# Optimization experiments

Measured on AMD Instinct MI355X. Metric: run time of the kernel, lower is better.

## Reference

```python
import jax, jax.numpy as jnp
import numpy as np

EMBED_DIM = 512
KDIM = 64
VDIM = 64


def setup_inputs() -> dict:
    key = jax.random.key(0)
    kx, kq, kk, kv = jax.random.split(key, 4)
    B, S = 4, 4096
    x = jax.random.normal(kx, (B, S, EMBED_DIM), dtype=jnp.float32)
    # nn.Linear(embed_dim, out) weight has shape [out, embed_dim]
    WQ = jax.random.normal(kq, (KDIM, EMBED_DIM), dtype=jnp.float32) * (EMBED_DIM ** -0.5)
    WK = jax.random.normal(kk, (KDIM, EMBED_DIM), dtype=jnp.float32) * (EMBED_DIM ** -0.5)
    WV = jax.random.normal(kv, (VDIM, EMBED_DIM), dtype=jnp.float32) * (EMBED_DIM ** -0.5)
    return {"x": x, "WQ": WQ, "WK": WK, "WV": WV}


def reference(x, WQ, WK, WV):
    # q,k: [B,S,kdim]; v: [B,S,vdim] (self-attention: x[0] is x[-1])
    q = jnp.einsum('bse,ke->bsk', x, WQ)
    k = jnp.einsum('bse,ke->bsk', x, WK)
    v = jnp.einsum('bse,ve->bsv', x, WV)
    scale = k.shape[-1] ** -0.5
    scores = jnp.einsum('bqk,bsk->bqs', q, k) * scale  # [B,S,S]
    # dropout p=0.0 -> identity; masked branch in source is a no-op (non-in-place masked_fill discarded)
    attn = jax.nn.softmax(scores, axis=-1)
    out = jnp.einsum('bqs,bsv->bqv', attn, v)  # [B,S,vdim]
    return out
```

## Files before the change

kernel.cpp:

```cpp
#include <hip/hip_runtime.h>

#define BATCH 4
#define SEQ   4096
#define EMB   512
#define HD    64

typedef __attribute__((ext_vector_type(8))) short short8;
typedef __attribute__((ext_vector_type(4))) float floatx4;

static __device__ __forceinline__ unsigned short f2bf(float f) {
  unsigned u = __builtin_bit_cast(unsigned, f);
  u += 0x7fffu + ((u >> 16) & 1u);
  return (unsigned short)(u >> 16);
}
static __device__ __forceinline__ float bf2f(unsigned short h) {
  unsigned u = ((unsigned)h) << 16;
  return __builtin_bit_cast(float, u);
}
static __device__ __forceinline__ unsigned pack_hi16(float lo, float hi) {
#if __has_builtin(__builtin_amdgcn_perm)
  return __builtin_amdgcn_perm(__builtin_bit_cast(unsigned, hi),
                               __builtin_bit_cast(unsigned, lo), 0x07060302u);
#else
  return (__builtin_bit_cast(unsigned, lo) >> 16) |
         (__builtin_bit_cast(unsigned, hi) & 0xffff0000u);
#endif
}
static __device__ __forceinline__ unsigned pack_f16(float a, float b) {
#if __has_builtin(__builtin_amdgcn_cvt_pkrtz)
  typedef __fp16 fp16v2 __attribute__((ext_vector_type(2)));
  fp16v2 h = __builtin_amdgcn_cvt_pkrtz(a, b);
  return __builtin_bit_cast(unsigned, h);
#else
  _Float16 ha = (_Float16)a, hb = (_Float16)b;
  return (unsigned)__builtin_bit_cast(unsigned short, ha) |
         ((unsigned)__builtin_bit_cast(unsigned short, hb) << 16);
#endif
}
static __device__ __forceinline__ float f16_to_f32(unsigned short bits) {
  _Float16 h = __builtin_bit_cast(_Float16, bits);
  return (float)h;
}

__global__ __launch_bounds__(256) void convw_kernel(
    const float* __restrict__ WQ, const float* __restrict__ WK,
    const float* __restrict__ WV, unsigned short* __restrict__ Wpk)
{
  int t = blockIdx.x * 256 + threadIdx.x;
  int p    = t >> 12;
  int w    = (t >> 10) & 3;
  int kc   = (t >> 6) & 15;
  int lane = t & 63;
  int lr = lane & 15, g = lane >> 4;
  const float* src = (p == 0) ? WQ : ((p == 1) ? WK : WV);
  const float4* s4 = (const float4*)(src + (16 * w + lr) * EMB + kc * 32 + 8 * g);
  float4 a = s4[0], b = s4[1];
  float vv[8] = {a.x, a.y, a.z, a.w, b.x, b.y, b.z, b.w};
  short8 o;
#pragma unroll
  for (int j = 0; j < 8; ++j) {
    unsigned short h = f2bf(vv[j]);
    o[j] = (p == 3) ? (short)f2bf(vv[j] - bf2f(h)) : (short)h;
  }
  *(short8*)(Wpk + (size_t)t * 8) = o;
}

__global__ __launch_bounds__(256) void proj_kernel(
    const float* __restrict__ x,
    const unsigned short* __restrict__ Wpk,
    unsigned short* __restrict__ Qb,
    unsigned short* __restrict__ Kb,
    unsigned short* __restrict__ VTb)
{
  const int tid  = threadIdx.x;
  const int lane = tid & 63;
  const int w    = tid >> 6;
  const int lr   = lane & 15, g = lane >> 4;
  const long rowBase = (long)blockIdx.x * 32;

  const float* xp[2];
  xp[0] = x + (rowBase + lr) * EMB + 8 * g;
  xp[1] = x + (rowBase + 16 + lr) * EMB + 8 * g;
  const unsigned short* const wb0 = Wpk + (size_t)(w * 16) * 512 + lane * 8;

  floatx4 accQ[2], accK[2], accV[2];
#pragma unroll
  for (int rt = 0; rt < 2; ++rt) {
    floatx4 z = {0.f, 0.f, 0.f, 0.f};
    accQ[rt] = z; accK[rt] = z; accV[rt] = z;
  }

#pragma unroll 4
  for (int kc = 0; kc < 16; ++kc) {
    const unsigned short* wb = wb0 + kc * 512;
    short8 wq  = *(const short8*)(wb);
    short8 wk  = *(const short8*)(wb + 32768);
    short8 wvh = *(const short8*)(wb + 2 * 32768);
    short8 wvl = *(const short8*)(wb + 3 * 32768);
#pragma unroll
    for (int rt = 0; rt < 2; ++rt) {
      const float4* p = (const float4*)(xp[rt] + kc * 32);
      float4 a = p[0], b = p[1];
      float vv[8] = {a.x, a.y, a.z, a.w, b.x, b.y, b.z, b.w};
      short8 xh, xl;
#pragma unroll
      for (int i = 0; i < 8; ++i) {
        unsigned short h = f2bf(vv[i]);
        xh[i] = (short)h;
        xl[i] = (short)f2bf(vv[i] - bf2f(h));
      }
      accQ[rt] = __builtin_amdgcn_mfma_f32_16x16x32_bf16(wq, xh, accQ[rt], 0, 0, 0);
      accK[rt] = __builtin_amdgcn_mfma_f32_16x16x32_bf16(wk, xh, accK[rt], 0, 0, 0);
      accV[rt] = __builtin_amdgcn_mfma_f32_16x16x32_bf16(xh, wvh, accV[rt], 0, 0, 0);
      accV[rt] = __builtin_amdgcn_mfma_f32_16x16x32_bf16(xl, wvh, accV[rt], 0, 0, 0);
      accV[rt] = __builtin_amdgcn_mfma_f32_16x16x32_bf16(xh, wvl, accV[rt], 0, 0, 0);
    }
  }

  const int bb  = (int)(rowBase >> 12);
  const int sIn = (int)(rowBase & 4095);
#pragma unroll
  for (int rt = 0; rt < 2; ++rt) {
    {
      long row = rowBase + 16 * rt + lr;
      int  col = 16 * w + 4 * g;
      ushort4 u; u.x = f2bf(accQ[rt][0]); u.y = f2bf(accQ[rt][1]);
      u.z = f2bf(accQ[rt][2]); u.w = f2bf(accQ[rt][3]);
      *(ushort4*)(Qb + row * HD + col) = u;
      ushort4 v; v.x = f2bf(accK[rt][0]); v.y = f2bf(accK[rt][1]);
      v.z = f2bf(accK[rt][2]); v.w = f2bf(accK[rt][3]);
      *(ushort4*)(Kb + row * HD + col) = v;
    }
    {
      long addr = ((long)(bb * 64 + 16 * w + lr)) * SEQ + sIn + 16 * rt + 4 * g;
      ushort4 u; u.x = f2bf(accV[rt][0]); u.y = f2bf(accV[rt][1]);
      u.z = f2bf(accV[rt][2]); u.w = f2bf(accV[rt][3]);
      *(ushort4*)(VTb + addr) = u;
    }
  }
}

#define PST 72

__global__ __launch_bounds__(256, 2) void flash_kernel(
    const unsigned short* __restrict__ Qb,
    const unsigned short* __restrict__ Kb,
    const unsigned short* __restrict__ VTb,
    unsigned short* __restrict__ Opart,
    float* __restrict__ Lpart)
{
  __shared__ __align__(16) unsigned short K0lds[64 * 64];
  __shared__ __align__(16) unsigned short V0lds[64 * 64];
  __shared__ __align__(16) unsigned short K1lds[64 * 64];
  __shared__ __align__(16) unsigned short V1lds[64 * 64];
  __shared__ __align__(16) unsigned short Plds[4][64 * PST];

  const int tid  = threadIdx.x;
  const int lane = tid & 63;
  const int w    = tid >> 6;
  const int lr   = lane & 15, g = lane >> 4;
  const int qb   = blockIdx.x >> 3;
  const int ks   = blockIdx.x & 7;
  const int bb   = qb >> 4;
  const long qrow0 = (long)qb * 256 + 64 * w;
  const int  kbase = ks * 512;

  const int koff0 = lr * 64 + 8 * ((    g) ^ (lr & 7));
  const int koff1 = lr * 64 + 8 * ((4 + g) ^ (lr & 7));
  const int voff0 = koff0, voff1 = koff1;
  const int pwoff = lr * PST + 4 * g;
  const int proff = lr * PST + 8 * g;
  unsigned short* const pw = &Plds[w][0];

  const int ci0  = tid;
  const int row0 = ci0 >> 3,        cc0 = (ci0 & 7) ^ (row0 & 7);
  const int ci1  = 256 + tid;
  const int row1 = ci1 >> 3,        cc1 = (ci1 & 7) ^ (row1 & 7);
  const unsigned short* const gK0 = Kb  + ((long)bb * SEQ + kbase + row0) * HD + cc0 * 8;
  const unsigned short* const gK1 = Kb  + ((long)bb * SEQ + kbase + row1) * HD + cc1 * 8;
  const unsigned short* const gV0 = VTb + ((long)bb * HD + row0) * SEQ + kbase + cc0 * 8;
  const unsigned short* const gV1 = VTb + ((long)bb * HD + row1) * SEQ + kbase + cc1 * 8;

  short8 qf[4][2];
#pragma unroll
  for (int qh = 0; qh < 4; ++qh)
#pragma unroll
    for (int ec = 0; ec < 2; ++ec)
      qf[qh][ec] = *(const short8*)(Qb + (qrow0 + 16 * qh + lr) * HD + ec * 32 + 8 * g);

  short8 onesb;
#pragma unroll
  for (int j = 0; j < 8; ++j) onesb[j] = (short)0x3F80;

  floatx4 accO[4][4], accL[4];
#pragma unroll
  for (int qh = 0; qh < 4; ++qh) {
    floatx4 z = {0.f,0.f,0.f,0.f};
    accL[qh] = z;
#pragma unroll
    for (int t = 0; t < 4; ++t) accO[qh][t] = z;
  }
  const float cp = 0.18033688011112042f;
  const float SH = 2.0f;

#define STAGE(kt_, KL, VL) do {                                               \
    const int ko_ = (kt_) * 64;                                               \
    __builtin_amdgcn_global_load_lds(                                         \
        (const __attribute__((address_space(1))) void*)(gK0 + (long)ko_ * HD),\
        (__attribute__((address_space(3))) void*)((KL) + ci0 * 8), 16, 0, 0); \
    __builtin_amdgcn_global_load_lds(                                         \
        (const __attribute__((address_space(1))) void*)(gV0 + ko_),           \
        (__attribute__((address_space(3))) void*)((VL) + ci0 * 8), 16, 0, 0); \
    __builtin_amdgcn_global_load_lds(                                         \
        (const __attribute__((address_space(1))) void*)(gK1 + (long)ko_ * HD),\
        (__attribute__((address_space(3))) void*)((KL) + ci1 * 8), 16, 0, 0); \
    __builtin_amdgcn_global_load_lds(                                         \
        (const __attribute__((address_space(1))) void*)(gV1 + ko_),           \
        (__attribute__((address_space(3))) void*)((VL) + ci1 * 8), 16, 0, 0); \
  } while (0)

#define COMPUTE(KL, VL) do {                                                  \
    short8 kf[2][4];                                                          \
    _Pragma("unroll")                                                         \
    for (int t = 0; t < 4; ++t) {                                             \
      kf[0][t] = *(const short8*)((KL) + koff0 + t * 1024);                   \
      kf[1][t] = *(const short8*)((KL) + koff1 + t * 1024);                   \
    }                                                                         \
    _Pragma("unroll")                                                         \
    for (int qh = 0; qh < 4; ++qh) {                                          \
      floatx4 s_[4];                                                          \
      _Pragma("unroll")                                                       \
      for (int t = 0; t < 4; ++t) { floatx4 z = {0.f,0.f,0.f,0.f}; s_[t] = z; } \
      _Pragma("unroll")                                                       \
      for (int ec = 0; ec < 2; ++ec)                                          \
        _Pragma("unroll")                                                     \
        for (int t = 0; t < 4; ++t)                                           \
          s_[t] = __builtin_amdgcn_mfma_f32_16x16x32_bf16(kf[ec][t], qf[qh][ec], s_[t], 0, 0, 0); \
      _Pragma("unroll")                                                       \
      for (int t = 0; t < 4; ++t) {                                           \
        float p0 = __builtin_amdgcn_exp2f(__builtin_fmaf(s_[t][0], cp, -SH)); \
        float p1 = __builtin_amdgcn_exp2f(__builtin_fmaf(s_[t][1], cp, -SH)); \
        float p2 = __builtin_amdgcn_exp2f(__builtin_fmaf(s_[t][2], cp, -SH)); \
        float p3 = __builtin_amdgcn_exp2f(__builtin_fmaf(s_[t][3], cp, -SH)); \
        uint2 u;                                                              \
        u.x = pack_hi16(p0, p1);                                              \
        u.y = pack_hi16(p2, p3);                                              \
        *(uint2*)(pw + pwoff + qh * (16 * PST) + t * 16) = u;                 \
      }                                                                       \
    }                                                                         \
    short8 vf[2][4];                                                          \
    _Pragma("unroll")                                                         \
    for (int t = 0; t < 4; ++t) {                                             \
      vf[0][t] = *(const short8*)((VL) + voff0 + t * 1024);                   \
      vf[1][t] = *(const short8*)((VL) + voff1 + t * 1024);                   \
    }                                                                         \
    _Pragma("unroll")                                                         \
    for (int qh = 0; qh < 4; ++qh)                                            \
      _Pragma("unroll")                                                       \
      for (int c = 0; c < 2; ++c) {                                           \
        short8 pf = *(const short8*)(pw + proff + qh * (16 * PST) + c * 32);  \
        accL[qh] = __builtin_amdgcn_mfma_f32_16x16x32_bf16(onesb, pf, accL[qh], 0, 0, 0); \
        _Pragma("unroll")                                                     \
        for (int t = 0; t < 4; ++t)                                           \
          accO[qh][t] = __builtin_amdgcn_mfma_f32_16x16x32_bf16(vf[c][t], pf, accO[qh][t], 0, 0, 0); \
      }                                                                       \
  } while (0)

  STAGE(0, K0lds, V0lds);
  for (int kt = 0; kt < 8; kt += 2) {
    __syncthreads();
    STAGE(kt + 1, K1lds, V1lds);
    COMPUTE(K0lds, V0lds);
    __syncthreads();
    if (kt + 2 < 8) STAGE(kt + 2, K0lds, V0lds);
    COMPUTE(K1lds, V1lds);
  }
#undef STAGE
#undef COMPUTE

  unsigned short* obase = Opart + (size_t)(qb * 8 + ks) * 256 * HD;
#pragma unroll
  for (int qh = 0; qh < 4; ++qh) {
    int qlocal = 64 * w + 16 * qh + lr;
#pragma unroll
    for (int t = 0; t < 4; ++t) {
      uint2 u;
      u.x = pack_f16(accO[qh][t][0], accO[qh][t][1]);
      u.y = pack_f16(accO[qh][t][2], accO[qh][t][3]);
      *(uint2*)(obase + qlocal * HD + 16 * t + 4 * g) = u;
    }
    if (g == 0) Lpart[(qb * 8 + ks) * 256 + qlocal] = accL[qh][0];
  }
}

__global__ __launch_bounds__(256) void combine_kernel(
    const unsigned short* __restrict__ Opart, const float* __restrict__ Lpart,
    float* __restrict__ out)
{
  int t   = blockIdx.x * 256 + threadIdx.x;
  int row = t >> 4;
  int d0  = (t & 15) * 4;
  int qb = row >> 8, qi = row & 255;
  float4 acc = {0.f, 0.f, 0.f, 0.f};
  float lt = 0.0f;
#pragma unroll
  for (int ks = 0; ks < 8; ++ks) {
    const unsigned short* p = Opart + ((size_t)(qb * 8 + ks) * 256 + qi) * HD + d0;
    ushort4 v = *(const ushort4*)p;
    acc.x += f16_to_f32(v.x);
    acc.y += f16_to_f32(v.y);
    acc.z += f16_to_f32(v.z);
    acc.w += f16_to_f32(v.w);
    lt += Lpart[(qb * 8 + ks) * 256 + qi];
  }
  float inv = 1.0f / lt;
  float4 o = {acc.x * inv, acc.y * inv, acc.z * inv, acc.w * inv};
  *(float4*)(out + (size_t)row * HD + d0) = o;
}

extern "C" void kernel_launch(void* const* d_in, const int* in_sizes, int n_in,
                              void* d_out, int out_size, void* d_ws, size_t ws_size,
                              hipStream_t stream) {
  const float* x  = (const float*)d_in[0];
  const float* WQ = (const float*)d_in[1];
  const float* WK = (const float*)d_in[2];
  const float* WV = (const float*)d_in[3];

  unsigned short* Qb  = (unsigned short*)d_ws;
  unsigned short* Kb  = Qb  + (size_t)BATCH * SEQ * HD;
  unsigned short* VTb = Kb  + (size_t)BATCH * SEQ * HD;
  unsigned short* Wpk = VTb + (size_t)BATCH * SEQ * HD;
  unsigned short* Opart = Wpk + 262144;
  float* Lpart = (float*)(Opart + (size_t)512 * 256 * HD);

  convw_kernel<<<64, 256, 0, stream>>>(WQ, WK, WV, Wpk);
  proj_kernel<<<(BATCH * SEQ) / 32, 256, 0, stream>>>(x, Wpk, Qb, Kb, VTb);
  flash_kernel<<<512, 256, 0, stream>>>(Qb, Kb, VTb, Opart, Lpart);
  combine_kernel<<<1024, 256, 0, stream>>>(Opart, Lpart, (float*)d_out);
}
```

Baseline: 125.5 us.

## Fold softmax scale into WQ, split keys 16 ways, single-buffer LDS

Folds the softmax scale (log2e/sqrt(d)) into WQ during weight conversion, so the inner loop does a bare exp2 with no fma or max-shift. The key split per query block doubles from 8 to 16 and the flash grid from 512 to 1024 blocks. LDS drops to single-buffered K/V so three blocks fit per CU, and the projection tile shrinks to 16 rows for more blocks. The cost is load latency no longer overlapped with compute, twice the partial-output traffic in combine, and dropping the -2 shift, which raises the chance of overflow or precision loss in the unnormalised exponentials.

```diff
diff --git a/kernel.cpp b/kernel.cpp
--- a/kernel.cpp
+++ b/kernel.cpp
@@ -41,6 +41,8 @@
   _Float16 h = __builtin_bit_cast(_Float16, bits);
   return (float)h;
 }
+
+#define CPSCALE 0.18033688011112042f
 
 __global__ __launch_bounds__(256) void convw_kernel(
     const float* __restrict__ WQ, const float* __restrict__ WK,
@@ -56,11 +58,13 @@
   const float4* s4 = (const float4*)(src + (16 * w + lr) * EMB + kc * 32 + 8 * g);
   float4 a = s4[0], b = s4[1];
   float vv[8] = {a.x, a.y, a.z, a.w, b.x, b.y, b.z, b.w};
+  const float sc = (p == 0) ? CPSCALE : 1.0f;
   short8 o;
 #pragma unroll
   for (int j = 0; j < 8; ++j) {
-    unsigned short h = f2bf(vv[j]);
-    o[j] = (p == 3) ? (short)f2bf(vv[j] - bf2f(h)) : (short)h;
+    float v = vv[j] * sc;
+    unsigned short h = f2bf(v);
+    o[j] = (p == 3) ? (short)f2bf(v - bf2f(h)) : (short)h;
   }
   *(short8*)(Wpk + (size_t)t * 8) = o;
 }
@@ -76,19 +80,12 @@
   const int lane = tid & 63;
   const int w    = tid >> 6;
   const int lr   = lane & 15, g = lane >> 4;
-  const long rowBase = (long)blockIdx.x * 32;
-
-  const float* xp[2];
-  xp[0] = x + (rowBase + lr) * EMB + 8 * g;
-  xp[1] = x + (rowBase + 16 + lr) * EMB + 8 * g;
+  const long rowBase = (long)blockIdx.x * 16;
+
+  const float* xp = x + (rowBase + lr) * EMB + 8 * g;
   const unsigned short* const wb0 = Wpk + (size_t)(w * 16) * 512 + lane * 8;
 
-  floatx4 accQ[2], accK[2], accV[2];
-#pragma unroll
-  for (int rt = 0; rt < 2; ++rt) {
-    floatx4 z = {0.f, 0.f, 0.f, 0.f};
-    accQ[rt] = z; accK[rt] = z; accV[rt] = z;
-  }
+  floatx4 accQ = {0.f,0.f,0.f,0.f}, accK = accQ, accV = accQ;
 
 #pragma unroll 4
   for (int kc = 0; kc < 16; ++kc) {
@@ -97,73 +94,65 @@
     short8 wk  = *(const short8*)(wb + 32768);
     short8 wvh = *(const short8*)(wb + 2 * 32768);
     short8 wvl = *(const short8*)(wb + 3 * 32768);
-#pragma unroll
-    for (int rt = 0; rt < 2; ++rt) {
-      const float4* p = (const float4*)(xp[rt] + kc * 32);
-      float4 a = p[0], b = p[1];
-      float vv[8] = {a.x, a.y, a.z, a.w, b.x, b.y, b.z, b.w};
-      short8 xh, xl;
-#pragma unroll
-      for (int i = 0; i < 8; ++i) {
-        unsigned short h = f2bf(vv[i]);
-        xh[i] = (short)h;
-        xl[i] = (short)f2bf(vv[i] - bf2f(h));
-      }
-      accQ[rt] = __builtin_amdgcn_mfma_f32_16x16x32_bf16(wq, xh, accQ[rt], 0, 0, 0);
-      accK[rt] = __builtin_amdgcn_mfma_f32_16x16x32_bf16(wk, xh, accK[rt], 0, 0, 0);
-      accV[rt] = __builtin_amdgcn_mfma_f32_16x16x32_bf16(xh, wvh, accV[rt], 0, 0, 0);
-      accV[rt] = __builtin_amdgcn_mfma_f32_16x16x32_bf16(xl, wvh, accV[rt], 0, 0, 0);
-      accV[rt] = __builtin_amdgcn_mfma_f32_16x16x32_bf16(xh, wvl, accV[rt], 0, 0, 0);
-    }
+    const float4* p = (const float4*)(xp + kc * 32);
+    float4 a = p[0], b = p[1];
+    float vv[8] = {a.x, a.y, a.z, a.w, b.x, b.y, b.z, b.w};
+    short8 xh, xl;
+#pragma unroll
+    for (int i = 0; i < 8; ++i) {
+      unsigned short h = f2bf(vv[i]);
+      xh[i] = (short)h;
+      xl[i] = (short)f2bf(vv[i] - bf2f(h));
+    }
+    accQ = __builtin_amdgcn_mfma_f32_16x16x32_bf16(wq, xh, accQ, 0, 0, 0);
+    accK = __builtin_amdgcn_mfma_f32_16x16x32_bf16(wk, xh, accK, 0, 0, 0);
+    accV = __builtin_amdgcn_mfma_f32_16x16x32_bf16(xh, wvh, accV, 0, 0, 0);
+    accV = __builtin_amdgcn_mfma_f32_16x16x32_bf16(xl, wvh, accV, 0, 0, 0);
+    accV = __builtin_amdgcn_mfma_f32_16x16x32_bf16(xh, wvl, accV, 0, 0, 0);
   }
 
   const int bb  = (int)(rowBase >> 12);
   const int sIn = (int)(rowBase & 4095);
-#pragma unroll
-  for (int rt = 0; rt < 2; ++rt) {
-    {
-      long row = rowBase + 16 * rt + lr;
-      int  col = 16 * w + 4 * g;
-      ushort4 u; u.x = f2bf(accQ[rt][0]); u.y = f2bf(accQ[rt][1]);
-      u.z = f2bf(accQ[rt][2]); u.w = f2bf(accQ[rt][3]);
-      *(ushort4*)(Qb + row * HD + col) = u;
-      ushort4 v; v.x = f2bf(accK[rt][0]); v.y = f2bf(accK[rt][1]);
-      v.z = f2bf(accK[rt][2]); v.w = f2bf(accK[rt][3]);
-      *(ushort4*)(Kb + row * HD + col) = v;
-    }
-    {
-      long addr = ((long)(bb * 64 + 16 * w + lr)) * SEQ + sIn + 16 * rt + 4 * g;
-      ushort4 u; u.x = f2bf(accV[rt][0]); u.y = f2bf(accV[rt][1]);
-      u.z = f2bf(accV[rt][2]); u.w = f2bf(accV[rt][3]);
-      *(ushort4*)(VTb + addr) = u;
-    }
+  {
+    long row = rowBase + lr;
+    int  col = 16 * w + 4 * g;
+    ushort4 u; u.x = f2bf(accQ[0]); u.y = f2bf(accQ[1]);
+    u.z = f2bf(accQ[2]); u.w = f2bf(accQ[3]);
+    *(ushort4*)(Qb + row * HD + col) = u;
+    ushort4 v; v.x = f2bf(accK[0]); v.y = f2bf(accK[1]);
+    v.z = f2bf(accK[2]); v.w = f2bf(accK[3]);
+    *(ushort4*)(Kb + row * HD + col) = v;
+  }
+  {
+    long addr = ((long)(bb * 64 + 16 * w + lr)) * SEQ + sIn + 4 * g;
+    ushort4 u; u.x = f2bf(accV[0]); u.y = f2bf(accV[1]);
+    u.z = f2bf(accV[2]); u.w = f2bf(accV[3]);
+    *(ushort4*)(VTb + addr) = u;
   }
 }
 
 #define PST 72
 
-__global__ __launch_bounds__(256, 2) void flash_kernel(
+__global__ __launch_bounds__(256, 3) void flash_kernel(
     const unsigned short* __restrict__ Qb,
     const unsigned short* __restrict__ Kb,
     const unsigned short* __restrict__ VTb,
     unsigned short* __restrict__ Opart,
     float* __restrict__ Lpart)
 {
-  __shared__ __align__(16) unsigned short K0lds[64 * 64];
-  __shared__ __align__(16) unsigned short V0lds[64 * 64];
-  __shared__ __align__(16) unsigned short K1lds[64 * 64];
-  __shared__ __align__(16) unsigned short V1lds[64 * 64];
+  __shared__ __align__(16) unsigned short Klds[64 * 64];
+  __shared__ __align__(16) unsigned short Vlds[64 * 64];
   __shared__ __align__(16) unsigned short Plds[4][64 * PST];
 
   const int tid  = threadIdx.x;
   const int lane = tid & 63;
   const int w    = tid >> 6;
   const int lr   = lane & 15, g = lane >> 4;
-  const int qb   = blockIdx.x >> 3;
-  const int ks   = blockIdx.x & 7;
+  const int qb   = blockIdx.x >> 4;
+  const int ks   = blockIdx.x & 15;
   const int bb   = qb >> 4;
   const long qrow0 = (long)qb * 256 + 64 * w;
-  const int  kbase = ks * 512;
+  const int  kbase = ks * 256;
 
   const int koff0 = lr * 64 + 8 * ((    g) ^ (lr & 7));
   const int koff1 = lr * 64 + 8 * ((4 + g) ^ (lr & 7));
@@ -200,85 +189,77 @@
 #pragma unroll
     for (int t = 0; t < 4; ++t) accO[qh][t] = z;
   }
-  const float cp = 0.18033688011112042f;
-  const float SH = 2.0f;
-
-#define STAGE(kt_, KL, VL) do {                                               \
+
+#define STAGE(kt_) do {                                                       \
     const int ko_ = (kt_) * 64;                                               \
     __builtin_amdgcn_global_load_lds(                                         \
         (const __attribute__((address_space(1))) void*)(gK0 + (long)ko_ * HD),\
-        (__attribute__((address_space(3))) void*)((KL) + ci0 * 8), 16, 0, 0); \
+        (__attribute__((address_space(3))) void*)(Klds + ci0 * 8), 16, 0, 0); \
     __builtin_amdgcn_global_load_lds(                                         \
         (const __attribute__((address_space(1))) void*)(gV0 + ko_),           \
-        (__attribute__((address_space(3))) void*)((VL) + ci0 * 8), 16, 0, 0); \
+        (__attribute__((address_space(3))) void*)(Vlds + ci0 * 8), 16, 0, 0); \
     __builtin_amdgcn_global_load_lds(                                         \
         (const __attribute__((address_space(1))) void*)(gK1 + (long)ko_ * HD),\
-        (__attribute__((address_space(3))) void*)((KL) + ci1 * 8), 16, 0, 0); \
+        (__attribute__((address_space(3))) void*)(Klds + ci1 * 8), 16, 0, 0); \
     __builtin_amdgcn_global_load_lds(                                         \
         (const __attribute__((address_space(1))) void*)(gV1 + ko_),           \
-        (__attribute__((address_space(3))) void*)((VL) + ci1 * 8), 16, 0, 0); \
+        (__attribute__((address_space(3))) void*)(Vlds + ci1 * 8), 16, 0, 0); \
   } while (0)
 
-#define COMPUTE(KL, VL) do {                                                  \
-    short8 kf[2][4];                                                          \
-    _Pragma("unroll")                                                         \
-    for (int t = 0; t < 4; ++t) {                                             \
-      kf[0][t] = *(const short8*)((KL) + koff0 + t * 1024);                   \
-      kf[1][t] = *(const short8*)((KL) + koff1 + t * 1024);                   \
-    }                                                                         \
-    _Pragma("unroll")                                                         \
-    for (int qh = 0; qh < 4; ++qh) {                                          \
-      floatx4 s_[4];                                                          \
-      _Pragma("unroll")                                                       \
-      for (int t = 0; t < 4; ++t) { floatx4 z = {0.f,0.f,0.f,0.f}; s_[t] = z; } \
-      _Pragma("unroll")                                                       \
-      for (int ec = 0; ec < 2; ++ec)                                          \
-        _Pragma("unroll")                                                     \
-        for (int t = 0; t < 4; ++t)                                           \
-          s_[t] = __builtin_amdgcn_mfma_f32_16x16x32_bf16(kf[ec][t], qf[qh][ec], s_[t], 0, 0, 0); \
-      _Pragma("unroll")                                                       \
-      for (int t = 0; t < 4; ++t) {                                           \
-        float p0 = __builtin_amdgcn_exp2f(__builtin_fmaf(s_[t][0], cp, -SH)); \
-        float p1 = __builtin_amdgcn_exp2f(__builtin_fmaf(s_[t][1], cp, -SH)); \
-        float p2 = __builtin_amdgcn_exp2f(__builtin_fmaf(s_[t][2], cp, -SH)); \
-        float p3 = __builtin_amdgcn_exp2f(__builtin_fmaf(s_[t][3], cp, -SH)); \
-        uint2 u;                                                              \
-        u.x = pack_hi16(p0, p1);                                              \
-        u.y = pack_hi16(p2, p3);                                              \
-        *(uint2*)(pw + pwoff + qh * (16 * PST) + t * 16) = u;                 \
-      }                                                                       \
-    }                                                                         \
-    short8 vf[2][4];                                                          \
-    _Pragma("unroll")                                                         \
-    for (int t = 0; t < 4; ++t) {                                             \
-      vf[0][t] = *(const short8*)((VL) + voff0 + t * 1024);                   \
-      vf[1][t] = *(const short8*)((VL) + voff1 + t * 1024);                   \
-    }                                                                         \
-    _Pragma("unroll")                                                         \
-    for (int qh = 0; qh < 4; ++qh)                                            \
-      _Pragma("unroll")                                                       \
-      for (int c = 0; c < 2; ++c) {                                           \
-        short8 pf = *(const short8*)(pw + proff + qh * (16 * PST) + c * 32);  \
-        accL[qh] = __builtin_amdgcn_mfma_f32_16x16x32_bf16(onesb, pf, accL[qh], 0, 0, 0); \
-        _Pragma("unroll")                                                     \
-        for (int t = 0; t < 4; ++t)                                           \
-          accO[qh][t] = __builtin_amdgcn_mfma_f32_16x16x32_bf16(vf[c][t], pf, accO[qh][t], 0, 0, 0); \
-      }                                                                       \
-  } while (0)
-
-  STAGE(0, K0lds, V0lds);
-  for (int kt = 0; kt < 8; kt += 2) {
+  STAGE(0);
+#pragma unroll
+  for (int kt = 0; kt < 4; ++kt) {
     __syncthreads();
-    STAGE(kt + 1, K1lds, V1lds);
-    COMPUTE(K0lds, V0lds);
+    short8 kf[2][4];
+#pragma unroll
+    for (int t = 0; t < 4; ++t) {
+      kf[0][t] = *(const short8*)(Klds + koff0 + t * 1024);
+      kf[1][t] = *(const short8*)(Klds + koff1 + t * 1024);
+    }
+#pragma unroll
+    for (int qh = 0; qh < 4; ++qh) {
+      floatx4 s_[4];
+#pragma unroll
+      for (int t = 0; t < 4; ++t) { floatx4 z = {0.f,0.f,0.f,0.f}; s_[t] = z; }
+#pragma unroll
+      for (int ec = 0; ec < 2; ++ec)
+#pragma unroll
+        for (int t = 0; t < 4; ++t)
+          s_[t] = __builtin_amdgcn_mfma_f32_16x16x32_bf16(kf[ec][t], qf[qh][ec], s_[t], 0, 0, 0);
+#pragma unroll
+      for (int t = 0; t < 4; ++t) {
+        float p0 = __builtin_amdgcn_exp2f(s_[t][0]);
+        float p1 = __builtin_amdgcn_exp2f(s_[t][1]);
+        float p2 = __builtin_amdgcn_exp2f(s_[t][2]);
+        float p3 = __builtin_amdgcn_exp2f(s_[t][3]);
+        uint2 u;
+        u.x = pack_hi16(p0, p1);
+        u.y = pack_hi16(p2, p3);
+        *(uint2*)(pw + pwoff + qh * (16 * PST) + t * 16) = u;
+      }
+    }
+    short8 vf[2][4];
+#pragma unroll
+    for (int t = 0; t < 4; ++t) {
+      vf[0][t] = *(const short8*)(Vlds + voff0 + t * 1024);
+      vf[1][t] = *(const short8*)(Vlds + voff1 + t * 1024);
+    }
+#pragma unroll
+    for (int qh = 0; qh < 4; ++qh)
+#pragma unroll
+      for (int c = 0; c < 2; ++c) {
+        short8 pf = *(const short8*)(pw + proff + qh * (16 * PST) + c * 32);
+        accL[qh] = __builtin_amdgcn_mfma_f32_16x16x32_bf16(onesb, pf, accL[qh], 0, 0, 0);
+#pragma unroll
+        for (int t = 0; t < 4; ++t)
+          accO[qh][t] = __builtin_amdgcn_mfma_f32_16x16x32_bf16(vf[c][t], pf, accO[qh][t], 0, 0, 0);
+      }
     __syncthreads();
-    if (kt + 2 < 8) STAGE(kt + 2, K0lds, V0lds);
-    COMPUTE(K1lds, V1lds);
+    if (kt + 1 < 4) STAGE(kt + 1);
   }
 #undef STAGE
-#undef COMPUTE
-
-  unsigned short* obase = Opart + (size_t)(qb * 8 + ks) * 256 * HD;
+
+  unsigned short* obase = Opart + (size_t)(qb * 16 + ks) * 256 * HD;
 #pragma unroll
   for (int qh = 0; qh < 4; ++qh) {
     int qlocal = 64 * w + 16 * qh + lr;
@@ -289,7 +270,7 @@
       u.y = pack_f16(accO[qh][t][2], accO[qh][t][3]);
       *(uint2*)(obase + qlocal * HD + 16 * t + 4 * g) = u;
     }
-    if (g == 0) Lpart[(qb * 8 + ks) * 256 + qlocal] = accL[qh][0];
+    if (g == 0) Lpart[(qb * 16 + ks) * 256 + qlocal] = accL[qh][0];
   }
 }
 
@@ -304,14 +285,14 @@
   float4 acc = {0.f, 0.f, 0.f, 0.f};
   float lt = 0.0f;
 #pragma unroll
-  for (int ks = 0; ks < 8; ++ks) {
-    const unsigned short* p = Opart + ((size_t)(qb * 8 + ks) * 256 + qi) * HD + d0;
+  for (int ks = 0; ks < 16; ++ks) {
+    const unsigned short* p = Opart + ((size_t)(qb * 16 + ks) * 256 + qi) * HD + d0;
     ushort4 v = *(const ushort4*)p;
     acc.x += f16_to_f32(v.x);
     acc.y += f16_to_f32(v.y);
     acc.z += f16_to_f32(v.z);
     acc.w += f16_to_f32(v.w);
-    lt += Lpart[(qb * 8 + ks) * 256 + qi];
+    lt += Lpart[(qb * 16 + ks) * 256 + qi];
   }
   float inv = 1.0f / lt;
   float4 o = {acc.x * inv, acc.y * inv, acc.z * inv, acc.w * inv};
@@ -331,10 +312,10 @@
   unsigned short* VTb = Kb  + (size_t)BATCH * SEQ * HD;
   unsigned short* Wpk = VTb + (size_t)BATCH * SEQ * HD;
   unsigned short* Opart = Wpk + 262144;
-  float* Lpart = (float*)(Opart + (size_t)512 * 256 * HD);
+  float* Lpart = (float*)(Opart + (size_t)1024 * 256 * HD);
 
   convw_kernel<<<64, 256, 0, stream>>>(WQ, WK, WV, Wpk);
-  proj_kernel<<<(BATCH * SEQ) / 32, 256, 0, stream>>>(x, Wpk, Qb, Kb, VTb);
-  flash_kernel<<<512, 256, 0, stream>>>(Qb, Kb, VTb, Opart, Lpart);
+  proj_kernel<<<(BATCH * SEQ) / 16, 256, 0, stream>>>(x, Wpk, Qb, Kb, VTb);
+  flash_kernel<<<1024, 256, 0, stream>>>(Qb, Kb, VTb, Opart, Lpart);
   combine_kernel<<<1024, 256, 0, stream>>>(Opart, Lpart, (float*)d_out);
 }
```

After: 152.7 us. +21.7%, slower.
